# Kernel tuning notes

Hardware: AMD Instinct MI355X
Metric: run time of the kernel (lower is better)

## Reference

```python
import jax, jax.numpy as jnp
import numpy as np

N_NODES = 100000
N_EDGES = 1600000
F_IN = 512
HIDDEN = 16
N_CLASSES = 40


def gcn_conv(x, edge_index, W, b, n_nodes):
    # PyG GCNConv: h = x @ W, add self-loops, sym-normalize, scatter-add, + bias
    h = x @ W  # [N, F_out]
    row, col = edge_index[0], edge_index[1]
    # add self-loops
    loop = jnp.arange(n_nodes, dtype=row.dtype)
    row = jnp.concatenate([row, loop])
    col = jnp.concatenate([col, loop])
    # degree of destination nodes (with self-loops)
    deg = jax.ops.segment_sum(jnp.ones_like(col, dtype=h.dtype), col,
                              num_segments=n_nodes)
    deg_inv_sqrt = jnp.where(deg > 0, jax.lax.rsqrt(deg), 0.0)
    norm = deg_inv_sqrt[row] * deg_inv_sqrt[col]  # [E+N]
    msg = h[row] * norm[:, None]  # gather + scale
    out = jax.ops.segment_sum(msg, col, num_segments=n_nodes)  # scatter-add
    return out + b


def setup_inputs() -> dict:
    key = jax.random.key(0)
    k1, k2, k3, k4 = jax.random.split(key, 4)
    x = jax.random.normal(k1, (N_NODES, F_IN), dtype=jnp.float32)
    edge_index = jax.random.randint(k2, (2, N_EDGES), 0, N_NODES, dtype=jnp.int64)
    # Glorot-style init for weights, zeros for biases (as PyG GCNConv)
    W1 = jax.random.normal(k3, (F_IN, HIDDEN), dtype=jnp.float32) / np.sqrt(F_IN)
    b1 = jnp.zeros((HIDDEN,), dtype=jnp.float32)
    W2 = jax.random.normal(k4, (HIDDEN, N_CLASSES), dtype=jnp.float32) / np.sqrt(HIDDEN)
    b2 = jnp.zeros((N_CLASSES,), dtype=jnp.float32)
    return {"x": x, "edge_index": edge_index, "W1": W1, "b1": b1,
            "W2": W2, "b2": b2}


def reference(x, edge_index, W1, b1, W2, b2):
    n = x.shape[0]
    h = gcn_conv(x, edge_index, W1, b1, n)
    h = jax.nn.relu(h)
    out = gcn_conv(h, edge_index, W2, b2, n)
    return out
```

## Files before the change

### kernel.cpp

```cpp
#include <hip/hip_runtime.h>

#define N_NODES 100000
#define N_EDGES 1600000
#define F_IN    512
#define HIDDEN  16
#define N_CLS   40

#define BSHIFT  7
#define BSIZE   128
#define NB      ((N_NODES + BSIZE - 1) / BSIZE)
#define NWGBIN  256
#define CHUNK   (N_EDGES / NWGBIN)

static_assert(N_EDGES % NWGBIN == 0, "chunking must be exact");

__global__ void k_zero(int* __restrict__ p, int n) {
    int i = blockIdx.x * blockDim.x + threadIdx.x;
    if (i < n) p[i] = 0;
}

__global__ __launch_bounds__(256) void k_binc(const int* __restrict__ ei,
                                              int* __restrict__ bucketCnt) {
    __shared__ int h[NB];
    int t = threadIdx.x;
    for (int b = t; b < NB; b += 256) h[b] = 0;
    __syncthreads();
    int start = blockIdx.x * CHUNK, end = start + CHUNK;
    for (int e = start + t; e < end; e += 256)
        atomicAdd(&h[ei[N_EDGES + e] >> BSHIFT], 1);
    __syncthreads();
    for (int b = t; b < NB; b += 256)
        if (h[b]) atomicAdd(&bucketCnt[b], h[b]);
}

__global__ __launch_bounds__(1024) void k_bscan(const int* __restrict__ bucketCnt,
                                                int* __restrict__ boff,
                                                int* __restrict__ cur) {
    __shared__ int s[1024];
    int t = threadIdx.x;
    int v = (t < NB) ? bucketCnt[t] : 0;
    s[t] = v; __syncthreads();
    for (int o = 1; o < 1024; o <<= 1) {
        int add = (t >= o) ? s[t - o] : 0;
        __syncthreads();
        s[t] += add;
        __syncthreads();
    }
    if (t < NB) { int ex = s[t] - v; boff[t] = ex; cur[t] = ex; }
    if (t == 0) boff[NB] = N_EDGES;
}

__global__ __launch_bounds__(256) void k_bfill(const int* __restrict__ ei,
                                               int* __restrict__ cur,
                                               int* __restrict__ binned) {
    __shared__ int lc[NB];
    int t = threadIdx.x;
    int start = blockIdx.x * CHUNK, end = start + CHUNK;
    for (int b = t; b < NB; b += 256) lc[b] = 0;
    __syncthreads();
    for (int e = start + t; e < end; e += 256)
        atomicAdd(&lc[ei[N_EDGES + e] >> BSHIFT], 1);
    __syncthreads();
    for (int b = t; b < NB; b += 256) {
        int c = lc[b];
        lc[b] = c ? atomicAdd(&cur[b], c) : 0;
    }
    __syncthreads();
    for (int e = start + t; e < end; e += 256) {
        int r = ei[e], c = ei[N_EDGES + e];
        int b = c >> BSHIFT;
        int pos = atomicAdd(&lc[b], 1);
        binned[pos] = r | ((c & (BSIZE - 1)) << 17);
    }
}

__global__ __launch_bounds__(256) void k_csr(const int* __restrict__ boff,
                                             const int* __restrict__ binned,
                                             int* __restrict__ csr,
                                             int* __restrict__ offsets,
                                             int* __restrict__ cnt,
                                             float* __restrict__ dis) {
    __shared__ int h[BSIZE];
    __shared__ int sc[BSIZE];
    __shared__ int curL[BSIZE];
    int t = threadIdx.x, b = blockIdx.x;
    if (t < BSIZE) h[t] = 0;
    __syncthreads();
    int s = boff[b], e = boff[b + 1];
    for (int i = s + t; i < e; i += 256)
        atomicAdd(&h[binned[i] >> 17], 1);
    __syncthreads();
    int v = (t < BSIZE) ? h[t] : 0;
    if (t < BSIZE) sc[t] = v;
    __syncthreads();
    for (int o = 1; o < BSIZE; o <<= 1) {
        int add = (t < BSIZE && t >= o) ? sc[t - o] : 0;
        __syncthreads();
        if (t < BSIZE) sc[t] += add;
        __syncthreads();
    }
    if (t < BSIZE) {
        int ex = s + sc[t] - v;
        curL[t] = ex;
        int node = b * BSIZE + t;
        if (node < N_NODES) {
            offsets[node] = ex;
            cnt[node]     = v;
            dis[node]     = rsqrtf(1.0f + (float)v);
        }
    }
    __syncthreads();
    for (int i = s + t; i < e; i += 256) {
        int p = binned[i];
        int pos = atomicAdd(&curL[p >> 17], 1);
        csr[pos] = p & 0x1FFFF;
    }
}

__global__ __launch_bounds__(256) void k_gemm1(
        const float* __restrict__ x, const float* __restrict__ W1,
        const float* __restrict__ dis, float* __restrict__ h1s) {
    __shared__ float sW[F_IN * 20];
    for (int idx = threadIdx.x; idx < F_IN * HIDDEN; idx += 256) {
        int k = idx >> 4, j = idx & 15;
        sW[k * 20 + j] = W1[idx];
    }
    __syncthreads();

    int t = threadIdx.x;
    int q = t & 3;
    int row0 = blockIdx.x * 128 + (t >> 2);
    int row1 = row0 + 64;
    bool ok0 = row0 < N_NODES, ok1 = row1 < N_NODES;
    const float* x0 = x + (size_t)row0 * F_IN;
    const float* x1 = x + (size_t)row1 * F_IN;

    float acc[2][16];
#pragma unroll
    for (int rr = 0; rr < 2; ++rr)
#pragma unroll
        for (int j = 0; j < 16; ++j) acc[rr][j] = 0.0f;

#pragma unroll 2
    for (int i = 0; i < 32; ++i) {
        int k0 = i * 16 + q * 4;
        float4 xv0 = ok0 ? *(const float4*)(x0 + k0) : float4{0, 0, 0, 0};
        float4 xv1 = ok1 ? *(const float4*)(x1 + k0) : float4{0, 0, 0, 0};
#pragma unroll
        for (int kk = 0; kk < 4; ++kk) {
            const float* wr = &sW[(k0 + kk) * 20];
            float4 w0 = *(const float4*)(wr);
            float4 w1 = *(const float4*)(wr + 4);
            float4 w2 = *(const float4*)(wr + 8);
            float4 w3 = *(const float4*)(wr + 12);
            float xs0 = (&xv0.x)[kk], xs1 = (&xv1.x)[kk];
            acc[0][0]  = fmaf(xs0, w0.x, acc[0][0]);   acc[1][0]  = fmaf(xs1, w0.x, acc[1][0]);
            acc[0][1]  = fmaf(xs0, w0.y, acc[0][1]);   acc[1][1]  = fmaf(xs1, w0.y, acc[1][1]);
            acc[0][2]  = fmaf(xs0, w0.z, acc[0][2]);   acc[1][2]  = fmaf(xs1, w0.z, acc[1][2]);
            acc[0][3]  = fmaf(xs0, w0.w, acc[0][3]);   acc[1][3]  = fmaf(xs1, w0.w, acc[1][3]);
            acc[0][4]  = fmaf(xs0, w1.x, acc[0][4]);   acc[1][4]  = fmaf(xs1, w1.x, acc[1][4]);
            acc[0][5]  = fmaf(xs0, w1.y, acc[0][5]);   acc[1][5]  = fmaf(xs1, w1.y, acc[1][5]);
            acc[0][6]  = fmaf(xs0, w1.z, acc[0][6]);   acc[1][6]  = fmaf(xs1, w1.z, acc[1][6]);
            acc[0][7]  = fmaf(xs0, w1.w, acc[0][7]);   acc[1][7]  = fmaf(xs1, w1.w, acc[1][7]);
            acc[0][8]  = fmaf(xs0, w2.x, acc[0][8]);   acc[1][8]  = fmaf(xs1, w2.x, acc[1][8]);
            acc[0][9]  = fmaf(xs0, w2.y, acc[0][9]);   acc[1][9]  = fmaf(xs1, w2.y, acc[1][9]);
            acc[0][10] = fmaf(xs0, w2.z, acc[0][10]);  acc[1][10] = fmaf(xs1, w2.z, acc[1][10]);
            acc[0][11] = fmaf(xs0, w2.w, acc[0][11]);  acc[1][11] = fmaf(xs1, w2.w, acc[1][11]);
            acc[0][12] = fmaf(xs0, w3.x, acc[0][12]);  acc[1][12] = fmaf(xs1, w3.x, acc[1][12]);
            acc[0][13] = fmaf(xs0, w3.y, acc[0][13]);  acc[1][13] = fmaf(xs1, w3.y, acc[1][13]);
            acc[0][14] = fmaf(xs0, w3.z, acc[0][14]);  acc[1][14] = fmaf(xs1, w3.z, acc[1][14]);
            acc[0][15] = fmaf(xs0, w3.w, acc[0][15]);  acc[1][15] = fmaf(xs1, w3.w, acc[1][15]);
        }
    }

#pragma unroll
    for (int rr = 0; rr < 2; ++rr) {
        float t16[16];
#pragma unroll
        for (int j = 0; j < 16; ++j)
            t16[j] = acc[rr][j] + __shfl_xor(acc[rr][j], 2);
        float k8[8];
#pragma unroll
        for (int j = 0; j < 8; ++j)
            k8[j] = (q & 2) ? t16[8 + j] : t16[j];
        float t8[8];
#pragma unroll
        for (int j = 0; j < 8; ++j)
            t8[j] = k8[j] + __shfl_xor(k8[j], 1);
#pragma unroll
        for (int j = 0; j < 4; ++j)
            acc[rr][j] = (q & 1) ? t8[4 + j] : t8[j];
    }

    if (ok0) {
        float d = dis[row0];
        *(float4*)(h1s + (size_t)row0 * HIDDEN + q * 4) =
            { acc[0][0] * d, acc[0][1] * d, acc[0][2] * d, acc[0][3] * d };
    }
    if (ok1) {
        float d = dis[row1];
        *(float4*)(h1s + (size_t)row1 * HIDDEN + q * 4) =
            { acc[1][0] * d, acc[1][1] * d, acc[1][2] * d, acc[1][3] * d };
    }
}

__global__ __launch_bounds__(256) void k_agg1(
        const int* __restrict__ offsets, const int* __restrict__ cnt,
        const int* __restrict__ csr, const float* __restrict__ dis,
        const float* __restrict__ b1,
        const float* __restrict__ h1s, float* __restrict__ g) {
    int t = blockIdx.x * 256 + threadIdx.x;
    int node = t >> 2;
    if (node >= N_NODES) return;
    int q = t & 3;
    int lanebase = (threadIdx.x & 63) & ~3;

    float4 acc = *(const float4*)(h1s + (size_t)node * HIDDEN + q * 4);
    int start = offsets[node];
    int n = cnt[node];
    int i = 0;
    for (; i + 4 <= n; i += 4) {
        int rv = csr[start + i + q];
#pragma unroll
        for (int j = 0; j < 4; ++j) {
            int r = __shfl(rv, lanebase + j);
            float4 v = *(const float4*)(h1s + (size_t)r * HIDDEN + q * 4);
            acc.x += v.x; acc.y += v.y; acc.z += v.z; acc.w += v.w;
        }
    }
    for (; i < n; ++i) {
        int r = csr[start + i];
        float4 v = *(const float4*)(h1s + (size_t)r * HIDDEN + q * 4);
        acc.x += v.x; acc.y += v.y; acc.z += v.z; acc.w += v.w;
    }
    float d = dis[node];
    float4 bq = *(const float4*)(b1 + q * 4);
    float4 r;
    r.x = fmaxf(fmaf(acc.x, d, bq.x), 0.0f) * d;
    r.y = fmaxf(fmaf(acc.y, d, bq.y), 0.0f) * d;
    r.z = fmaxf(fmaf(acc.z, d, bq.z), 0.0f) * d;
    r.w = fmaxf(fmaf(acc.w, d, bq.w), 0.0f) * d;
    *(float4*)(g + (size_t)node * HIDDEN + q * 4) = r;
}

__global__ __launch_bounds__(256) void k_agg2(
        const int* __restrict__ offsets, const int* __restrict__ cnt,
        const int* __restrict__ csr, const float* __restrict__ dis,
        const float* __restrict__ W2, const float* __restrict__ b2,
        const float* __restrict__ g, float* __restrict__ out) {
    __shared__ float sW[HIDDEN * N_CLS];
    __shared__ float sb2[N_CLS];
    __shared__ float sAgg[64][HIDDEN + 1];
    int t = threadIdx.x;
    for (int i = t; i < HIDDEN * N_CLS; i += 256) sW[i] = W2[i];
    if (t < N_CLS) sb2[t] = b2[t];

    int gt = blockIdx.x * 256 + t;
    int node = gt >> 2;
    int q = t & 3;
    int ln = t >> 2;
    int lanebase = (t & 63) & ~3;

    if (node < N_NODES) {
        float4 acc = *(const float4*)(g + (size_t)node * HIDDEN + q * 4);
        int start = offsets[node];
        int n = cnt[node];
        int i = 0;
        for (; i + 4 <= n; i += 4) {
            int rv = csr[start + i + q];
#pragma unroll
            for (int j = 0; j < 4; ++j) {
                int r = __shfl(rv, lanebase + j);
                float4 v = *(const float4*)(g + (size_t)r * HIDDEN + q * 4);
                acc.x += v.x; acc.y += v.y; acc.z += v.z; acc.w += v.w;
            }
        }
        for (; i < n; ++i) {
            int r = csr[start + i];
            float4 v = *(const float4*)(g + (size_t)r * HIDDEN + q * 4);
            acc.x += v.x; acc.y += v.y; acc.z += v.z; acc.w += v.w;
        }
        float d = dis[node];
        sAgg[ln][q*4+0] = acc.x * d;
        sAgg[ln][q*4+1] = acc.y * d;
        sAgg[ln][q*4+2] = acc.z * d;
        sAgg[ln][q*4+3] = acc.w * d;
    }
    __syncthreads();
    if (node >= N_NODES) return;

    float a[HIDDEN];
#pragma unroll
    for (int j = 0; j < HIDDEN; ++j) a[j] = sAgg[ln][j];

    int c0 = q * 10;
    float o[10];
#pragma unroll
    for (int k = 0; k < 10; ++k) o[k] = sb2[c0 + k];
#pragma unroll
    for (int j = 0; j < HIDDEN; ++j) {
        float aj = a[j];
        const float* wr = &sW[j * N_CLS + c0];
#pragma unroll
        for (int k = 0; k < 10; ++k) o[k] = fmaf(aj, wr[k], o[k]);
    }
    float* op = out + (size_t)node * N_CLS + c0;
#pragma unroll
    for (int k = 0; k < 10; ++k) op[k] = o[k];
}

extern "C" void kernel_launch(void* const* d_in, const int* in_sizes, int n_in,
                              void* d_out, int out_size, void* d_ws, size_t ws_size,
                              hipStream_t stream) {
    const float* x  = (const float*)d_in[0];
    const int*   ei = (const int*)d_in[1];
    const float* W1 = (const float*)d_in[2];
    const float* b1 = (const float*)d_in[3];
    const float* W2 = (const float*)d_in[4];
    const float* b2 = (const float*)d_in[5];
    float* out = (float*)d_out;

    char* w = (char*)d_ws;
    int*   bucketCnt = (int*)w;    w += 784 * 4;
    int*   boff      = (int*)w;    w += 784 * 4;
    int*   cur       = (int*)w;    w += 784 * 4;
    int*   offsets   = (int*)w;    w += (size_t)N_NODES * 4;
    int*   cnt       = (int*)w;    w += (size_t)N_NODES * 4;
    float* dis       = (float*)w;  w += (size_t)N_NODES * 4;
    int*   binned    = (int*)w;    w += (size_t)N_EDGES * 4;
    int*   csr       = (int*)w;    w += (size_t)N_EDGES * 4;
    float* h1s       = (float*)w;  w += (size_t)N_NODES * HIDDEN * 4;
    float* g         = (float*)w;

    const int gGemm = (N_NODES + 127) / 128;
    const int gAgg  = (N_NODES * 4 + 255) / 256;

    k_zero <<<(NB + 255) / 256, 256, 0, stream>>>(bucketCnt, NB);
    k_binc <<<NWGBIN, 256, 0, stream>>>(ei, bucketCnt);
    k_bscan<<<1, 1024, 0, stream>>>(bucketCnt, boff, cur);
    k_bfill<<<NWGBIN, 256, 0, stream>>>(ei, cur, binned);
    k_csr  <<<NB, 256, 0, stream>>>(boff, binned, csr, offsets, cnt, dis);
    k_gemm1<<<gGemm, 256, 0, stream>>>(x, W1, dis, h1s);
    k_agg1 <<<gAgg, 256, 0, stream>>>(offsets, cnt, csr, dis, b1, h1s, g);
    k_agg2 <<<gAgg, 256, 0, stream>>>(offsets, cnt, csr, dis, W2, b2, g, out);
}
```

Measured before the change: 451.2 us.

## Pad CSR rows to multiples of four and gather neighbors with int4 index loads

CSR neighbor lists are padded to 4-aligned segments filled with a dummy node index. That index points at an extra zeroed feature row in h1s and in g. Both aggregation kernels then read indices as int4 and issue eight independent float4 gathers per iteration, replacing the shuffle-based index broadcast and the scalar tail loop. The first GEMM also changes its shared-memory W1 stride from 20 to 17, clamps out-of-range rows instead of branching on loads, and unrolls further. The stride-17 float4 shared reads are misaligned, which may break or slow those loads. The padding adds extra gather work and a larger CSR buffer.

```diff
diff --git a/kernel.cpp b/kernel.cpp
--- a/kernel.cpp
+++ b/kernel.cpp
@@ -11,12 +11,15 @@
 #define NB      ((N_NODES + BSIZE - 1) / BSIZE)
 #define NWGBIN  256
 #define CHUNK   (N_EDGES / NWGBIN)
+#define CSR_CAP (N_EDGES + NB * 512 + 64)
 
 static_assert(N_EDGES % NWGBIN == 0, "chunking must be exact");
 
-__global__ void k_zero(int* __restrict__ p, int n) {
+__global__ void k_zero(int* __restrict__ bucketCnt,
+                       float* __restrict__ h1pad, float* __restrict__ gpad) {
     int i = blockIdx.x * blockDim.x + threadIdx.x;
-    if (i < n) p[i] = 0;
+    if (i < NB) bucketCnt[i] = 0;
+    if (i < HIDDEN) { h1pad[i] = 0.0f; gpad[i] = 0.0f; }
 }
 
 __global__ __launch_bounds__(256) void k_binc(const int* __restrict__ ei,
@@ -90,8 +93,9 @@
     for (int i = s + t; i < e; i += 256)
         atomicAdd(&h[binned[i] >> 17], 1);
     __syncthreads();
-    int v = (t < BSIZE) ? h[t] : 0;
-    if (t < BSIZE) sc[t] = v;
+    int v  = (t < BSIZE) ? h[t] : 0;
+    int vp = (v + 3) & ~3;
+    if (t < BSIZE) sc[t] = vp;
     __syncthreads();
     for (int o = 1; o < BSIZE; o <<= 1) {
         int add = (t < BSIZE && t >= o) ? sc[t - o] : 0;
@@ -99,8 +103,9 @@
         if (t < BSIZE) sc[t] += add;
         __syncthreads();
     }
+    int base = ((s + 3) & ~3) + b * 512;
     if (t < BSIZE) {
-        int ex = s + sc[t] - v;
+        int ex = base + sc[t] - vp;
         curL[t] = ex;
         int node = b * BSIZE + t;
         if (node < N_NODES) {
@@ -108,6 +113,7 @@
             cnt[node]     = v;
             dis[node]     = rsqrtf(1.0f + (float)v);
         }
+        for (int j = v; j < vp; ++j) csr[ex + j] = N_NODES;
     }
     __syncthreads();
     for (int i = s + t; i < e; i += 256) {
@@ -120,10 +126,10 @@
 __global__ __launch_bounds__(256) void k_gemm1(
         const float* __restrict__ x, const float* __restrict__ W1,
         const float* __restrict__ dis, float* __restrict__ h1s) {
-    __shared__ float sW[F_IN * 20];
+    __shared__ float sW[F_IN * 17];
     for (int idx = threadIdx.x; idx < F_IN * HIDDEN; idx += 256) {
         int k = idx >> 4, j = idx & 15;
-        sW[k * 20 + j] = W1[idx];
+        sW[k * 17 + j] = W1[idx];
     }
     __syncthreads();
 
@@ -132,8 +138,10 @@
     int row0 = blockIdx.x * 128 + (t >> 2);
     int row1 = row0 + 64;
     bool ok0 = row0 < N_NODES, ok1 = row1 < N_NODES;
-    const float* x0 = x + (size_t)row0 * F_IN;
-    const float* x1 = x + (size_t)row1 * F_IN;
+    int r0c = ok0 ? row0 : (N_NODES - 1);
+    int r1c = ok1 ? row1 : (N_NODES - 1);
+    const float* x0 = x + (size_t)r0c * F_IN;
+    const float* x1 = x + (size_t)r1c * F_IN;
 
     float acc[2][16];
 #pragma unroll
@@ -141,14 +149,14 @@
 #pragma unroll
         for (int j = 0; j < 16; ++j) acc[rr][j] = 0.0f;
 
-#pragma unroll 2
+#pragma unroll 4
     for (int i = 0; i < 32; ++i) {
         int k0 = i * 16 + q * 4;
-        float4 xv0 = ok0 ? *(const float4*)(x0 + k0) : float4{0, 0, 0, 0};
-        float4 xv1 = ok1 ? *(const float4*)(x1 + k0) : float4{0, 0, 0, 0};
+        float4 xv0 = *(const float4*)(x0 + k0);
+        float4 xv1 = *(const float4*)(x1 + k0);
 #pragma unroll
         for (int kk = 0; kk < 4; ++kk) {
-            const float* wr = &sW[(k0 + kk) * 20];
+            const float* wr = &sW[(k0 + kk) * 17];
             float4 w0 = *(const float4*)(wr);
             float4 w1 = *(const float4*)(wr + 4);
             float4 w2 = *(const float4*)(wr + 8);
@@ -213,25 +221,36 @@
     int node = t >> 2;
     if (node >= N_NODES) return;
     int q = t & 3;
-    int lanebase = (threadIdx.x & 63) & ~3;
 
     float4 acc = *(const float4*)(h1s + (size_t)node * HIDDEN + q * 4);
-    int start = offsets[node];
-    int n = cnt[node];
+    const int4* cp = (const int4*)(csr + offsets[node]);
+    int n4 = (cnt[node] + 3) >> 2;
     int i = 0;
-    for (; i + 4 <= n; i += 4) {
-        int rv = csr[start + i + q];
-#pragma unroll
-        for (int j = 0; j < 4; ++j) {
-            int r = __shfl(rv, lanebase + j);
-            float4 v = *(const float4*)(h1s + (size_t)r * HIDDEN + q * 4);
-            acc.x += v.x; acc.y += v.y; acc.z += v.z; acc.w += v.w;
-        }
-    }
-    for (; i < n; ++i) {
-        int r = csr[start + i];
-        float4 v = *(const float4*)(h1s + (size_t)r * HIDDEN + q * 4);
-        acc.x += v.x; acc.y += v.y; acc.z += v.z; acc.w += v.w;
+    for (; i + 2 <= n4; i += 2) {
+        int4 c0 = cp[i], c1 = cp[i + 1];
+        float4 v0 = *(const float4*)(h1s + (size_t)c0.x * HIDDEN + q * 4);
+        float4 v1 = *(const float4*)(h1s + (size_t)c0.y * HIDDEN + q * 4);
+        float4 v2 = *(const float4*)(h1s + (size_t)c0.z * HIDDEN + q * 4);
+        float4 v3 = *(const float4*)(h1s + (size_t)c0.w * HIDDEN + q * 4);
+        float4 v4 = *(const float4*)(h1s + (size_t)c1.x * HIDDEN + q * 4);
+        float4 v5 = *(const float4*)(h1s + (size_t)c1.y * HIDDEN + q * 4);
+        float4 v6 = *(const float4*)(h1s + (size_t)c1.z * HIDDEN + q * 4);
+        float4 v7 = *(const float4*)(h1s + (size_t)c1.w * HIDDEN + q * 4);
+        acc.x += v0.x + v1.x + v2.x + v3.x + v4.x + v5.x + v6.x + v7.x;
+        acc.y += v0.y + v1.y + v2.y + v3.y + v4.y + v5.y + v6.y + v7.y;
+        acc.z += v0.z + v1.z + v2.z + v3.z + v4.z + v5.z + v6.z + v7.z;
+        acc.w += v0.w + v1.w + v2.w + v3.w + v4.w + v5.w + v6.w + v7.w;
+    }
+    if (i < n4) {
+        int4 c0 = cp[i];
+        float4 v0 = *(const float4*)(h1s + (size_t)c0.x * HIDDEN + q * 4);
+        float4 v1 = *(const float4*)(h1s + (size_t)c0.y * HIDDEN + q * 4);
+        float4 v2 = *(const float4*)(h1s + (size_t)c0.z * HIDDEN + q * 4);
+        float4 v3 = *(const float4*)(h1s + (size_t)c0.w * HIDDEN + q * 4);
+        acc.x += v0.x + v1.x + v2.x + v3.x;
+        acc.y += v0.y + v1.y + v2.y + v3.y;
+        acc.z += v0.z + v1.z + v2.z + v3.z;
+        acc.w += v0.w + v1.w + v2.w + v3.w;
     }
     float d = dis[node];
     float4 bq = *(const float4*)(b1 + q * 4);
@@ -259,26 +278,37 @@
     int node = gt >> 2;
     int q = t & 3;
     int ln = t >> 2;
-    int lanebase = (t & 63) & ~3;
 
     if (node < N_NODES) {
         float4 acc = *(const float4*)(g + (size_t)node * HIDDEN + q * 4);
-        int start = offsets[node];
-        int n = cnt[node];
+        const int4* cp = (const int4*)(csr + offsets[node]);
+        int n4 = (cnt[node] + 3) >> 2;
         int i = 0;
-        for (; i + 4 <= n; i += 4) {
-            int rv = csr[start + i + q];
-#pragma unroll
-            for (int j = 0; j < 4; ++j) {
-                int r = __shfl(rv, lanebase + j);
-                float4 v = *(const float4*)(g + (size_t)r * HIDDEN + q * 4);
-                acc.x += v.x; acc.y += v.y; acc.z += v.z; acc.w += v.w;
-            }
+        for (; i + 2 <= n4; i += 2) {
+            int4 c0 = cp[i], c1 = cp[i + 1];
+            float4 v0 = *(const float4*)(g + (size_t)c0.x * HIDDEN + q * 4);
+            float4 v1 = *(const float4*)(g + (size_t)c0.y * HIDDEN + q * 4);
+            float4 v2 = *(const float4*)(g + (size_t)c0.z * HIDDEN + q * 4);
+            float4 v3 = *(const float4*)(g + (size_t)c0.w * HIDDEN + q * 4);
+            float4 v4 = *(const float4*)(g + (size_t)c1.x * HIDDEN + q * 4);
+            float4 v5 = *(const float4*)(g + (size_t)c1.y * HIDDEN + q * 4);
+            float4 v6 = *(const float4*)(g + (size_t)c1.z * HIDDEN + q * 4);
+            float4 v7 = *(const float4*)(g + (size_t)c1.w * HIDDEN + q * 4);
+            acc.x += v0.x + v1.x + v2.x + v3.x + v4.x + v5.x + v6.x + v7.x;
+            acc.y += v0.y + v1.y + v2.y + v3.y + v4.y + v5.y + v6.y + v7.y;
+            acc.z += v0.z + v1.z + v2.z + v3.z + v4.z + v5.z + v6.z + v7.z;
+            acc.w += v0.w + v1.w + v2.w + v3.w + v4.w + v5.w + v6.w + v7.w;
         }
-        for (; i < n; ++i) {
-            int r = csr[start + i];
-            float4 v = *(const float4*)(g + (size_t)r * HIDDEN + q * 4);
-            acc.x += v.x; acc.y += v.y; acc.z += v.z; acc.w += v.w;
+        if (i < n4) {
+            int4 c0 = cp[i];
+            float4 v0 = *(const float4*)(g + (size_t)c0.x * HIDDEN + q * 4);
+            float4 v1 = *(const float4*)(g + (size_t)c0.y * HIDDEN + q * 4);
+            float4 v2 = *(const float4*)(g + (size_t)c0.z * HIDDEN + q * 4);
+            float4 v3 = *(const float4*)(g + (size_t)c0.w * HIDDEN + q * 4);
+            acc.x += v0.x + v1.x + v2.x + v3.x;
+            acc.y += v0.y + v1.y + v2.y + v3.y;
+            acc.z += v0.z + v1.z + v2.z + v3.z;
+            acc.w += v0.w + v1.w + v2.w + v3.w;
         }
         float d = dis[node];
         sAgg[ln][q*4+0] = acc.x * d;
@@ -321,21 +351,22 @@
     float* out = (float*)d_out;
 
     char* w = (char*)d_ws;
-    int*   bucketCnt = (int*)w;    w += 784 * 4;
-    int*   boff      = (int*)w;    w += 784 * 4;
-    int*   cur       = (int*)w;    w += 784 * 4;
+    int*   bucketCnt = (int*)w;    w += 1024 * 4;
+    int*   boff      = (int*)w;    w += 1024 * 4;
+    int*   cur       = (int*)w;    w += 1024 * 4;
     int*   offsets   = (int*)w;    w += (size_t)N_NODES * 4;
     int*   cnt       = (int*)w;    w += (size_t)N_NODES * 4;
-    float* dis       = (float*)w;  w += (size_t)N_NODES * 4;
+    float* dis       = (float*)w;  w += (size_t)N_NODES * 4 + 64;
     int*   binned    = (int*)w;    w += (size_t)N_EDGES * 4;
-    int*   csr       = (int*)w;    w += (size_t)N_EDGES * 4;
-    float* h1s       = (float*)w;  w += (size_t)N_NODES * HIDDEN * 4;
+    int*   csr       = (int*)w;    w += (size_t)CSR_CAP * 4;
+    float* h1s       = (float*)w;  w += (size_t)(N_NODES + 1) * HIDDEN * 4;
     float* g         = (float*)w;
 
     const int gGemm = (N_NODES + 127) / 128;
     const int gAgg  = (N_NODES * 4 + 255) / 256;
 
-    k_zero <<<(NB + 255) / 256, 256, 0, stream>>>(bucketCnt, NB);
+    k_zero <<<(NB + 255) / 256, 256, 0, stream>>>(bucketCnt,
+                h1s + (size_t)N_NODES * HIDDEN, g + (size_t)N_NODES * HIDDEN);
     k_binc <<<NWGBIN, 256, 0, stream>>>(ei, bucketCnt);
     k_bscan<<<1, 1024, 0, stream>>>(bucketCnt, boff, cur);
     k_bfill<<<NWGBIN, 256, 0, stream>>>(ei, cur, binned);
```

After: 506.1 us. 12.2% more time.
